# Optimization experiments

Measured on AMD Instinct MI355X. Metric: run time of the kernel, lower is better.

## Reference

```python
import jax, jax.numpy as jnp
import numpy as np

N_HEAD = 12

def fillnan(x):
    return jnp.nan_to_num(x, nan=0.0, posinf=0.0, neginf=0.0)

def setup_inputs() -> dict:
    key = jax.random.key(0)
    k1, k2, k3 = jax.random.split(key, 3)
    B, T, C = 2, 2048, 768
    x = jax.random.normal(k1, (B, T, C), dtype=jnp.float32)
    W_attn = jax.random.normal(k2, (3 * C, C), dtype=jnp.float32) * 0.02
    W_proj = jax.random.normal(k3, (C, C), dtype=jnp.float32) * 0.02
    return {"x": x, "W_attn": W_attn, "W_proj": W_proj}

def reference(x, W_attn, W_proj):
    B, T, C = x.shape
    H = N_HEAD
    D = C // H
    # qkv projection (torch Linear: x @ W^T), then nan-sanitize
    qkv = fillnan(jnp.einsum('btc,fc->btf', x, W_attn))  # [B,T,3C]
    q, k, v = jnp.split(qkv, 3, axis=-1)
    # [B,T,C] -> [B,H,T,D]
    q = q.reshape(B, T, H, D).transpose(0, 2, 1, 3)
    k = k.reshape(B, T, H, D).transpose(0, 2, 1, 3)
    v = v.reshape(B, T, H, D).transpose(0, 2, 1, 3)
    scale = 1.0 / np.sqrt(D).astype(np.float32)
    att = jnp.einsum('bhqd,bhkd->bhqk', q, k) * scale  # [B,H,T,T]
    att = fillnan(att)
    causal = jnp.tril(jnp.ones((T, T), dtype=bool))
    att = jnp.where(causal[None, None], att, -jnp.inf)
    att = jax.nn.softmax(att, axis=-1)
    att = fillnan(att)
    y = jnp.einsum('bhqk,bhkd->bhqd', att, v)  # [B,H,T,D]
    y = fillnan(y)
    y = y.transpose(0, 2, 1, 3).reshape(B, T, C)
    y = fillnan(jnp.einsum('btc,fc->btf', y, W_proj))
    return y
```

## Files before the change

### kernel.cpp

```cpp
#include <hip/hip_runtime.h>

typedef __attribute__((ext_vector_type(8))) short bf16x8;
typedef __attribute__((ext_vector_type(4))) float f32x4;

__device__ __forceinline__ unsigned short f2b(float f) {
  union { float f; unsigned u; } v; v.f = f;
  return (unsigned short)((v.u + 0x7FFFu + ((v.u >> 16) & 1u)) >> 16);
}
__device__ __forceinline__ unsigned short f2b_fast(float f) {
  union { float f; unsigned u; } v; v.f = f;
  return (unsigned short)((v.u + 0x8000u) >> 16);
}

#define XN4   786432
#define WAN4  442368
#define WPN4  147456
__global__ void cvt_all(const float* __restrict__ x, const float* __restrict__ Wa,
                        const float* __restrict__ Wp,
                        unsigned short* __restrict__ xb, unsigned short* __restrict__ Wab,
                        unsigned short* __restrict__ Wpb) {
  int i = blockIdx.x * 256 + threadIdx.x;
  const float* src; unsigned short* dst; int off;
  if (i < XN4)            { src = x;  dst = xb;  off = i; }
  else if (i < XN4 + WAN4){ src = Wa; dst = Wab; off = i - XN4; }
  else                    { src = Wp; dst = Wpb; off = i - XN4 - WAN4; }
  float4 f = reinterpret_cast<const float4*>(src)[off];
  ushort4 o;
  o.x = f2b(f.x); o.y = f2b(f.y); o.z = f2b(f.z); o.w = f2b(f.w);
  reinterpret_cast<ushort4*>(dst)[off] = o;
}

__global__ __launch_bounds__(256, 2)
void gemm_qkv(const unsigned short* __restrict__ A,
              const unsigned short* __restrict__ Bm,
              unsigned short* __restrict__ qb,
              unsigned short* __restrict__ kb_,
              unsigned short* __restrict__ vt) {
  __shared__ unsigned short As[2][128 * 64];
  __shared__ unsigned short Bs[2][128 * 64];
  const int K = 768;
  int tid = threadIdx.x;
  int wave = tid >> 6, lane = tid & 63;
  int quad = lane >> 4, l16 = lane & 15;
  int m0 = blockIdx.x * 128, n0 = blockIdx.y * 128;
  int wm = (wave & 1) * 64, wn = (wave >> 1) * 64;
  bool vswap = (n0 >= 1536);

  int srow = lane >> 3;
  int scol = ((lane & 7) ^ srow) << 3;

  auto stage = [&](int k0, int buf) {
#pragma unroll
    for (int i = 0; i < 4; ++i) {
      int r = wave * 32 + i * 8;
      __builtin_amdgcn_global_load_lds(
          (const __attribute__((address_space(1))) unsigned int*)(A + (size_t)(m0 + r + srow) * K + k0 + scol),
          (__attribute__((address_space(3))) unsigned int*)(&As[buf][r * 64]), 16, 0, 0);
      __builtin_amdgcn_global_load_lds(
          (const __attribute__((address_space(1))) unsigned int*)(Bm + (size_t)(n0 + r + srow) * K + k0 + scol),
          (__attribute__((address_space(3))) unsigned int*)(&Bs[buf][r * 64]), 16, 0, 0);
    }
  };

  f32x4 acc[4][4] = {};
  stage(0, 0);
  int cur = 0;

  for (int k0 = 0; k0 < K; k0 += 64) {
    __syncthreads();
    if (k0 + 64 < K) stage(k0 + 64, cur ^ 1);
#pragma unroll
    for (int kb = 0; kb < 2; ++kb) {
      int ch = (((kb << 2) | quad) ^ (l16 & 7)) << 3;
      bf16x8 af[4], bf[4];
#pragma unroll
      for (int i = 0; i < 4; ++i)
        af[i] = *reinterpret_cast<const bf16x8*>(&As[cur][(wm + i * 16 + l16) * 64 + ch]);
#pragma unroll
      for (int j = 0; j < 4; ++j)
        bf[j] = *reinterpret_cast<const bf16x8*>(&Bs[cur][(wn + j * 16 + l16) * 64 + ch]);
      if (!vswap) {
#pragma unroll
        for (int i = 0; i < 4; ++i)
#pragma unroll
          for (int j = 0; j < 4; ++j)
            acc[i][j] = __builtin_amdgcn_mfma_f32_16x16x32_bf16(af[i], bf[j], acc[i][j], 0, 0, 0);
      } else {
#pragma unroll
        for (int i = 0; i < 4; ++i)
#pragma unroll
          for (int j = 0; j < 4; ++j)
            acc[i][j] = __builtin_amdgcn_mfma_f32_16x16x32_bf16(bf[j], af[i], acc[i][j], 0, 0, 0);
      }
    }
    cur ^= 1;
  }

  const float scale2 = 0.125f * 1.44269504089f;
  if (!vswap) {
#pragma unroll
    for (int i = 0; i < 4; ++i) {
      int mbase = m0 + wm + i * 16 + quad * 4;
#pragma unroll
      for (int j = 0; j < 4; ++j) {
        int f = n0 + wn + j * 16 + l16;
        int which = f / 768;
        int f2 = f - which * 768;
        int h = f2 >> 6, d = f2 & 63;
#pragma unroll
        for (int r = 0; r < 4; ++r) {
          int m = mbase + r;
          int b = m >> 11, t = m & 2047;
          int bh = b * 12 + h;
          if (which == 0) qb[((size_t)(bh * 2048 + t)) * 64 + d] = f2b(acc[i][j][r] * scale2);
          else            kb_[((size_t)(bh * 2048 + t)) * 64 + d] = f2b(acc[i][j][r]);
        }
      }
    }
  } else {
#pragma unroll
    for (int j = 0; j < 4; ++j) {
      int fbase = n0 + wn + j * 16 + quad * 4 - 1536;
#pragma unroll
      for (int i = 0; i < 4; ++i) {
        int t_g = m0 + wm + i * 16 + l16;
        int b = t_g >> 11, t = t_g & 2047;
#pragma unroll
        for (int r = 0; r < 4; ++r) {
          int f2 = fbase + r;
          int h = f2 >> 6, d = f2 & 63;
          int bh = b * 12 + h;
          vt[((size_t)(bh * 64 + d)) * 2048 + t] = f2b(acc[i][j][r]);
        }
      }
    }
  }
}

#define CK 256

__global__ __launch_bounds__(256, 3)
void attn_part(const unsigned short* __restrict__ Qb,
               const unsigned short* __restrict__ Kb,
               const unsigned short* __restrict__ Vt,
               float* __restrict__ Oacc, float* __restrict__ Lacc) {
  __shared__ unsigned short Ks[2][64 * 64];
  __shared__ unsigned short Vs[2][64 * 64];
  __shared__ unsigned short P[4 * 32 * 64];
  const int T = 2048, D = 64;
  int wave = threadIdx.x >> 6, lane = threadIdx.x & 63;
  int quad = lane >> 4, l16 = lane & 15;

  int flat = blockIdx.x;
  int xcd = flat & 7;
  int ix = flat >> 3;
  int bh = xcd * 3 + ix / 72;
  int r = ix % 72;
  int b = 15;
#pragma unroll
  for (int i = 0; i < 16; ++i) {
    int nb = (i >> 1) + 1;
    if (r < nb) { b = i; break; }
    r -= nb;
  }
  int c = r;
  int q0 = b * 128;
  int qrow = q0 + wave * 32;
  int kbeg = c * CK;
  int kend = kbeg + CK; if (kend > q0 + 128) kend = q0 + 128;

  const unsigned short* Qp = Qb + (size_t)bh * T * D;
  const unsigned short* Kp = Kb + (size_t)bh * T * D;
  const unsigned short* Vp = Vt + (size_t)bh * D * T;
  unsigned short* Pw = P + wave * 32 * 64;

  int srow = lane >> 3;
  int scol = ((lane & 7) ^ srow) << 3;

  auto stage = [&](int k0, int buf) {
#pragma unroll
    for (int i = 0; i < 2; ++i) {
      int rr = wave * 16 + i * 8;
      __builtin_amdgcn_global_load_lds(
          (const __attribute__((address_space(1))) unsigned int*)(Kp + (size_t)(k0 + rr + srow) * D + scol),
          (__attribute__((address_space(3))) unsigned int*)(&Ks[buf][rr * 64]), 16, 0, 0);
      __builtin_amdgcn_global_load_lds(
          (const __attribute__((address_space(1))) unsigned int*)(Vp + (size_t)(rr + srow) * T + k0 + scol),
          (__attribute__((address_space(3))) unsigned int*)(&Vs[buf][rr * 64]), 16, 0, 0);
    }
  };

  bf16x8 aq[2][2];
#pragma unroll
  for (int qi = 0; qi < 2; ++qi)
#pragma unroll
    for (int cc = 0; cc < 2; ++cc)
      aq[qi][cc] = *reinterpret_cast<const bf16x8*>(
          Qp + (qrow + qi * 16 + l16) * D + cc * 32 + quad * 8);

  bf16x8 ones;
#pragma unroll
  for (int e = 0; e < 8; ++e) ones[e] = (short)0x3F80;

  f32x4 o[2][4] = {};
  f32x4 lacc[2] = {};
  int pswr = (l16 & 7) ^ (l16 >> 3);

  stage(kbeg, 0);
  int cur = 0;

  for (int k0 = kbeg; k0 < kend; k0 += 64) {
    __syncthreads();
    if (k0 + 64 < kend) stage(k0 + 64, cur ^ 1);

    if (k0 <= qrow + 31) {
      f32x4 sacc[2][4] = {};
#pragma unroll
      for (int nt = 0; nt < 4; ++nt) {
        bf16x8 bk0 = *reinterpret_cast<const bf16x8*>(&Ks[cur][(nt * 16 + l16) * 64 + ((quad ^ (l16 & 7)) << 3)]);
        bf16x8 bk1 = *reinterpret_cast<const bf16x8*>(&Ks[cur][(nt * 16 + l16) * 64 + (((4 | quad) ^ (l16 & 7)) << 3)]);
#pragma unroll
        for (int qi = 0; qi < 2; ++qi) {
          sacc[qi][nt] = __builtin_amdgcn_mfma_f32_16x16x32_bf16(aq[qi][0], bk0, sacc[qi][nt], 0, 0, 0);
          sacc[qi][nt] = __builtin_amdgcn_mfma_f32_16x16x32_bf16(aq[qi][1], bk1, sacc[qi][nt], 0, 0, 0);
        }
      }

      if (k0 + 63 > qrow) {
#pragma unroll
        for (int qi = 0; qi < 2; ++qi)
#pragma unroll
          for (int nt = 0; nt < 4; ++nt) {
            int col = k0 + nt * 16 + l16;
#pragma unroll
            for (int rr = 0; rr < 4; ++rr) {
              int row = qrow + qi * 16 + quad * 4 + rr;
              sacc[qi][nt][rr] = (col <= row) ? sacc[qi][nt][rr] : -1e30f;
            }
          }
      }
#pragma unroll
      for (int qi = 0; qi < 2; ++qi)
#pragma unroll
        for (int nt = 0; nt < 4; ++nt)
#pragma unroll
          for (int rr = 0; rr < 4; ++rr)
            sacc[qi][nt][rr] = exp2f(sacc[qi][nt][rr]);

#pragma unroll
      for (int qi = 0; qi < 2; ++qi)
#pragma unroll
        for (int rr = 0; rr < 4; ++rr) {
          int prow = qi * 16 + quad * 4 + rr;
          int psw = (prow & 7) ^ ((prow >> 3) & 1);
#pragma unroll
          for (int nt = 0; nt < 4; ++nt)
            Pw[prow * 64 + (((nt * 2 + (l16 >> 3)) ^ psw) << 3) + (l16 & 7)] = f2b_fast(sacc[qi][nt][rr]);
        }
      __asm__ volatile("s_waitcnt lgkmcnt(0)" ::: "memory");

      bf16x8 vf[4][2];
#pragma unroll
      for (int dt = 0; dt < 4; ++dt) {
        vf[dt][0] = *reinterpret_cast<const bf16x8*>(&Vs[cur][(dt * 16 + l16) * 64 + ((quad ^ (l16 & 7)) << 3)]);
        vf[dt][1] = *reinterpret_cast<const bf16x8*>(&Vs[cur][(dt * 16 + l16) * 64 + (((4 | quad) ^ (l16 & 7)) << 3)]);
      }
#pragma unroll
      for (int qi = 0; qi < 2; ++qi) {
        bf16x8 ap0 = *reinterpret_cast<const bf16x8*>(Pw + (qi * 16 + l16) * 64 + ((quad ^ pswr) << 3));
        bf16x8 ap1 = *reinterpret_cast<const bf16x8*>(Pw + (qi * 16 + l16) * 64 + (((4 | quad) ^ pswr) << 3));
#pragma unroll
        for (int dt = 0; dt < 4; ++dt) {
          o[qi][dt] = __builtin_amdgcn_mfma_f32_16x16x32_bf16(ap0, vf[dt][0], o[qi][dt], 0, 0, 0);
          o[qi][dt] = __builtin_amdgcn_mfma_f32_16x16x32_bf16(ap1, vf[dt][1], o[qi][dt], 0, 0, 0);
        }
        lacc[qi] = __builtin_amdgcn_mfma_f32_16x16x32_bf16(ap0, ones, lacc[qi], 0, 0, 0);
        lacc[qi] = __builtin_amdgcn_mfma_f32_16x16x32_bf16(ap1, ones, lacc[qi], 0, 0, 0);
      }
      __asm__ volatile("" ::: "memory");
    }
    cur ^= 1;
  }

#pragma unroll
  for (int qi = 0; qi < 2; ++qi)
#pragma unroll
    for (int dt = 0; dt < 4; ++dt)
#pragma unroll
      for (int rr = 0; rr < 4; ++rr) {
        int row = qrow + qi * 16 + quad * 4 + rr;
        atomicAdd(&Oacc[((size_t)(bh * T + row)) * 64 + dt * 16 + l16], o[qi][dt][rr]);
      }
  if (l16 == 0) {
#pragma unroll
    for (int qi = 0; qi < 2; ++qi)
#pragma unroll
      for (int rr = 0; rr < 4; ++rr)
        atomicAdd(&Lacc[bh * T + qrow + qi * 16 + quad * 4 + rr], lacc[qi][rr]);
  }
}

__global__ __launch_bounds__(256, 2)
void gemm_proj(const float* __restrict__ Oacc, const float* __restrict__ Lacc,
               const unsigned short* __restrict__ Wpb, float* __restrict__ out) {
  __shared__ unsigned short As[2][64 * 64];
  __shared__ unsigned short Bs[2][128 * 64];
  int tid = threadIdx.x;
  int wave = tid >> 6, lane = tid & 63;
  int quad = lane >> 4, l16 = lane & 15;
  int m0 = blockIdx.x * 64, n0 = blockIdx.y * 128;
  int wm = (wave & 1) * 32, wn = (wave >> 1) * 64;

  int srow = lane >> 3;
  int scol = ((lane & 7) ^ srow) << 3;

  int arow = tid >> 2;
  int acg = (tid & 3) * 2;
  int t_g = m0 + arow;
  int bb = t_g >> 11, tt = t_g & 2047;
  int asw = arow & 7;

  auto stageB = [&](int k0, int buf) {
#pragma unroll
    for (int i = 0; i < 4; ++i) {
      int r = wave * 32 + i * 8;
      __builtin_amdgcn_global_load_lds(
          (const __attribute__((address_space(1))) unsigned int*)(Wpb + (size_t)(n0 + r + srow) * 768 + k0 + scol),
          (__attribute__((address_space(3))) unsigned int*)(&Bs[buf][r * 64]), 16, 0, 0);
    }
  };
  auto loadA = [&](int k0, float4* a, float& rl) {
    int h = k0 >> 6;
    const float* arp = Oacc + ((size_t)((bb * 12 + h) * 2048 + tt)) * 64 + acg * 8;
    rl = 1.0f / Lacc[(bb * 12 + h) * 2048 + tt];
    a[0] = reinterpret_cast<const float4*>(arp)[0];
    a[1] = reinterpret_cast<const float4*>(arp)[1];
    a[2] = reinterpret_cast<const float4*>(arp)[2];
    a[3] = reinterpret_cast<const float4*>(arp)[3];
  };
  auto writeA = [&](const float4* a, float rl, int buf) {
    bf16x8 p0, p1;
    p0[0] = (short)f2b(a[0].x * rl); p0[1] = (short)f2b(a[0].y * rl);
    p0[2] = (short)f2b(a[0].z * rl); p0[3] = (short)f2b(a[0].w * rl);
    p0[4] = (short)f2b(a[1].x * rl); p0[5] = (short)f2b(a[1].y * rl);
    p0[6] = (short)f2b(a[1].z * rl); p0[7] = (short)f2b(a[1].w * rl);
    p1[0] = (short)f2b(a[2].x * rl); p1[1] = (short)f2b(a[2].y * rl);
    p1[2] = (short)f2b(a[2].z * rl); p1[3] = (short)f2b(a[2].w * rl);
    p1[4] = (short)f2b(a[3].x * rl); p1[5] = (short)f2b(a[3].y * rl);
    p1[6] = (short)f2b(a[3].z * rl); p1[7] = (short)f2b(a[3].w * rl);
    *reinterpret_cast<bf16x8*>(&As[buf][arow * 64 + ((acg ^ asw) << 3)]) = p0;
    *reinterpret_cast<bf16x8*>(&As[buf][arow * 64 + (((acg + 1) ^ asw) << 3)]) = p1;
  };

  f32x4 acc[2][4] = {};

  float4 aP[4], aN[4];
  float rlP, rlN;
  stageB(0, 0);
  loadA(0, aP, rlP);
  loadA(64, aN, rlN);
  writeA(aP, rlP, 0);
  int cur = 0;

  for (int k0 = 0; k0 < 768; k0 += 64) {
    __syncthreads();
    if (k0 + 64 < 768) {
      stageB(k0 + 64, cur ^ 1);
      writeA(aN, rlN, cur ^ 1);
      if (k0 + 128 < 768) loadA(k0 + 128, aN, rlN);
    }
#pragma unroll
    for (int kb = 0; kb < 2; ++kb) {
      int ch = (((kb << 2) | quad) ^ (l16 & 7)) << 3;
      bf16x8 af[2], bf[4];
#pragma unroll
      for (int i = 0; i < 2; ++i)
        af[i] = *reinterpret_cast<const bf16x8*>(&As[cur][(wm + i * 16 + l16) * 64 + ch]);
#pragma unroll
      for (int j = 0; j < 4; ++j)
        bf[j] = *reinterpret_cast<const bf16x8*>(&Bs[cur][(wn + j * 16 + l16) * 64 + ch]);
#pragma unroll
      for (int i = 0; i < 2; ++i)
#pragma unroll
        for (int j = 0; j < 4; ++j)
          acc[i][j] = __builtin_amdgcn_mfma_f32_16x16x32_bf16(af[i], bf[j], acc[i][j], 0, 0, 0);
    }
    cur ^= 1;
  }

#pragma unroll
  for (int i = 0; i < 2; ++i) {
    int mbase = m0 + wm + i * 16 + quad * 4;
#pragma unroll
    for (int j = 0; j < 4; ++j) {
      int col = n0 + wn + j * 16 + l16;
#pragma unroll
      for (int r = 0; r < 4; ++r)
        out[(size_t)(mbase + r) * 768 + col] = acc[i][j][r];
    }
  }
}

extern "C" void kernel_launch(void* const* d_in, const int* in_sizes, int n_in,
                              void* d_out, int out_size, void* d_ws, size_t ws_size,
                              hipStream_t stream) {
  const float* x  = (const float*)d_in[0];
  const float* Wa = (const float*)d_in[1];
  const float* Wp = (const float*)d_in[2];
  float* out = (float*)d_out;

  unsigned short* ws = (unsigned short*)d_ws;
  unsigned short* xb  = ws;
  unsigned short* Wab = xb  + 3145728;
  unsigned short* Wpb = Wab + 1769472;
  unsigned short* Qb  = Wpb + 589824;
  unsigned short* Kb  = Qb  + 3145728;
  unsigned short* Vt  = Kb  + 3145728;
  float*          Oacc = (float*)(Vt + 3145728);
  float*          Lacc = Oacc + 3145728;

  hipMemsetAsync(Oacc, 0, (3145728 + 49152) * sizeof(float), stream);

  cvt_all<<<(XN4 + WAN4 + WPN4) / 256, 256, 0, stream>>>(x, Wa, Wp, xb, Wab, Wpb);

  gemm_qkv<<<dim3(32, 18), 256, 0, stream>>>(xb, Wab, Qb, Kb, Vt);

  attn_part<<<1728, 256, 0, stream>>>(Qb, Kb, Vt, Oacc, Lacc);

  gemm_proj<<<dim3(64, 6), 256, 0, stream>>>(Oacc, Lacc, Wpb, out);
}
```

Before: 180.8 us.

## Restructure attention into independent per-wave 16-row tasks with direct global K/V loads

The attention kernel now gives each wave its own 16-query-row × 256-key chunk. Each wave loads K and V fragments straight from global memory into registers, which removes the shared-memory staging, double buffering and block-wide barriers. Blocks become 512 threads with 8 independent waves, so causal work is spread more finely and there is no intra-block sync. The memset of the accumulators is folded into the conversion kernel to save a launch. In exchange, K/V reuse across waves through LDS is lost, and there are more global loads and atomics per output row.

```diff
diff --git a/kernel.cpp b/kernel.cpp
--- a/kernel.cpp
+++ b/kernel.cpp
@@ -15,11 +15,18 @@
 #define XN4   786432
 #define WAN4  442368
 #define WPN4  147456
+#define CVTN  1376256
+#define ZN4   798720
 __global__ void cvt_all(const float* __restrict__ x, const float* __restrict__ Wa,
                         const float* __restrict__ Wp,
                         unsigned short* __restrict__ xb, unsigned short* __restrict__ Wab,
-                        unsigned short* __restrict__ Wpb) {
+                        unsigned short* __restrict__ Wpb, float* __restrict__ Oacc) {
   int i = blockIdx.x * 256 + threadIdx.x;
+  if (i >= CVTN) {
+    int z = i - CVTN;
+    reinterpret_cast<float4*>(Oacc)[z] = make_float4(0.f, 0.f, 0.f, 0.f);
+    return;
+  }
   const float* src; unsigned short* dst; int off;
   if (i < XN4)            { src = x;  dst = xb;  off = i; }
   else if (i < XN4 + WAN4){ src = Wa; dst = Wab; off = i - XN4; }
@@ -137,166 +144,114 @@
   }
 }
 
-#define CK 256
-
-__global__ __launch_bounds__(256, 3)
+#define AT_LDP 72
+
+__global__ __launch_bounds__(512, 4)
 void attn_part(const unsigned short* __restrict__ Qb,
                const unsigned short* __restrict__ Kb,
                const unsigned short* __restrict__ Vt,
                float* __restrict__ Oacc, float* __restrict__ Lacc) {
-  __shared__ unsigned short Ks[2][64 * 64];
-  __shared__ unsigned short Vs[2][64 * 64];
-  __shared__ unsigned short P[4 * 32 * 64];
+  __shared__ unsigned short P[8 * 16 * AT_LDP];
   const int T = 2048, D = 64;
   int wave = threadIdx.x >> 6, lane = threadIdx.x & 63;
   int quad = lane >> 4, l16 = lane & 15;
 
-  int flat = blockIdx.x;
-  int xcd = flat & 7;
-  int ix = flat >> 3;
+  int blk = blockIdx.x;
+  int xcd = blk & 7;
+  int ix = blk >> 3;
   int bh = xcd * 3 + ix / 72;
-  int r = ix % 72;
-  int b = 15;
-#pragma unroll
-  for (int i = 0; i < 16; ++i) {
-    int nb = (i >> 1) + 1;
-    if (r < nb) { b = i; break; }
-    r -= nb;
-  }
-  int c = r;
-  int q0 = b * 128;
-  int qrow = q0 + wave * 32;
-  int kbeg = c * CK;
-  int kend = kbeg + CK; if (kend > q0 + 128) kend = q0 + 128;
+  int r = (ix % 72) * 8 + wave;
+  int qt = 0, c = 0;
+#pragma unroll
+  for (int G = 0; G < 8; ++G) {
+    int cnt = 16 * (G + 1);
+    if (r >= cnt) { r -= cnt; }
+    else { qt = G * 16 + r / (G + 1); c = r % (G + 1); break; }
+  }
+  int qrow = qt * 16;
+  int kbeg = c * 256;
+  int kend = kbeg + 256; if (kend > qrow + 16) kend = qrow + 16;
 
   const unsigned short* Qp = Qb + (size_t)bh * T * D;
   const unsigned short* Kp = Kb + (size_t)bh * T * D;
   const unsigned short* Vp = Vt + (size_t)bh * D * T;
-  unsigned short* Pw = P + wave * 32 * 64;
-
-  int srow = lane >> 3;
-  int scol = ((lane & 7) ^ srow) << 3;
-
-  auto stage = [&](int k0, int buf) {
-#pragma unroll
-    for (int i = 0; i < 2; ++i) {
-      int rr = wave * 16 + i * 8;
-      __builtin_amdgcn_global_load_lds(
-          (const __attribute__((address_space(1))) unsigned int*)(Kp + (size_t)(k0 + rr + srow) * D + scol),
-          (__attribute__((address_space(3))) unsigned int*)(&Ks[buf][rr * 64]), 16, 0, 0);
-      __builtin_amdgcn_global_load_lds(
-          (const __attribute__((address_space(1))) unsigned int*)(Vp + (size_t)(rr + srow) * T + k0 + scol),
-          (__attribute__((address_space(3))) unsigned int*)(&Vs[buf][rr * 64]), 16, 0, 0);
-    }
-  };
-
-  bf16x8 aq[2][2];
-#pragma unroll
-  for (int qi = 0; qi < 2; ++qi)
-#pragma unroll
-    for (int cc = 0; cc < 2; ++cc)
-      aq[qi][cc] = *reinterpret_cast<const bf16x8*>(
-          Qp + (qrow + qi * 16 + l16) * D + cc * 32 + quad * 8);
+  unsigned short* Pw = P + wave * 16 * AT_LDP;
+
+  bf16x8 aq[2];
+#pragma unroll
+  for (int cc = 0; cc < 2; ++cc)
+    aq[cc] = *reinterpret_cast<const bf16x8*>(Qp + (qrow + l16) * D + cc * 32 + quad * 8);
 
   bf16x8 ones;
 #pragma unroll
   for (int e = 0; e < 8; ++e) ones[e] = (short)0x3F80;
 
-  f32x4 o[2][4] = {};
-  f32x4 lacc[2] = {};
-  int pswr = (l16 & 7) ^ (l16 >> 3);
-
-  stage(kbeg, 0);
-  int cur = 0;
+  f32x4 o[4] = {};
+  f32x4 lacc = {};
 
   for (int k0 = kbeg; k0 < kend; k0 += 64) {
-    __syncthreads();
-    if (k0 + 64 < kend) stage(k0 + 64, cur ^ 1);
-
-    if (k0 <= qrow + 31) {
-      f32x4 sacc[2][4] = {};
-#pragma unroll
-      for (int nt = 0; nt < 4; ++nt) {
-        bf16x8 bk0 = *reinterpret_cast<const bf16x8*>(&Ks[cur][(nt * 16 + l16) * 64 + ((quad ^ (l16 & 7)) << 3)]);
-        bf16x8 bk1 = *reinterpret_cast<const bf16x8*>(&Ks[cur][(nt * 16 + l16) * 64 + (((4 | quad) ^ (l16 & 7)) << 3)]);
-#pragma unroll
-        for (int qi = 0; qi < 2; ++qi) {
-          sacc[qi][nt] = __builtin_amdgcn_mfma_f32_16x16x32_bf16(aq[qi][0], bk0, sacc[qi][nt], 0, 0, 0);
-          sacc[qi][nt] = __builtin_amdgcn_mfma_f32_16x16x32_bf16(aq[qi][1], bk1, sacc[qi][nt], 0, 0, 0);
-        }
+    bf16x8 kf[4][2];
+#pragma unroll
+    for (int nt = 0; nt < 4; ++nt) {
+      const unsigned short* kr = Kp + (size_t)(k0 + nt * 16 + l16) * D + quad * 8;
+      kf[nt][0] = *reinterpret_cast<const bf16x8*>(kr);
+      kf[nt][1] = *reinterpret_cast<const bf16x8*>(kr + 32);
+    }
+    f32x4 sacc[4] = {};
+#pragma unroll
+    for (int nt = 0; nt < 4; ++nt) {
+      sacc[nt] = __builtin_amdgcn_mfma_f32_16x16x32_bf16(aq[0], kf[nt][0], sacc[nt], 0, 0, 0);
+      sacc[nt] = __builtin_amdgcn_mfma_f32_16x16x32_bf16(aq[1], kf[nt][1], sacc[nt], 0, 0, 0);
+    }
+    bf16x8 vf[4][2];
+#pragma unroll
+    for (int dt = 0; dt < 4; ++dt) {
+      const unsigned short* vr = Vp + (size_t)(dt * 16 + l16) * T + k0 + quad * 8;
+      vf[dt][0] = *reinterpret_cast<const bf16x8*>(vr);
+      vf[dt][1] = *reinterpret_cast<const bf16x8*>(vr + 32);
+    }
+
+#pragma unroll
+    for (int nt = 0; nt < 4; ++nt) {
+      int col = k0 + nt * 16 + l16;
+#pragma unroll
+      for (int rr = 0; rr < 4; ++rr) {
+        int row = qrow + quad * 4 + rr;
+        float s = (col <= row) ? sacc[nt][rr] : -1e30f;
+        sacc[nt][rr] = exp2f(s);
       }
-
-      if (k0 + 63 > qrow) {
-#pragma unroll
-        for (int qi = 0; qi < 2; ++qi)
-#pragma unroll
-          for (int nt = 0; nt < 4; ++nt) {
-            int col = k0 + nt * 16 + l16;
-#pragma unroll
-            for (int rr = 0; rr < 4; ++rr) {
-              int row = qrow + qi * 16 + quad * 4 + rr;
-              sacc[qi][nt][rr] = (col <= row) ? sacc[qi][nt][rr] : -1e30f;
-            }
-          }
-      }
-#pragma unroll
-      for (int qi = 0; qi < 2; ++qi)
-#pragma unroll
-        for (int nt = 0; nt < 4; ++nt)
-#pragma unroll
-          for (int rr = 0; rr < 4; ++rr)
-            sacc[qi][nt][rr] = exp2f(sacc[qi][nt][rr]);
-
-#pragma unroll
-      for (int qi = 0; qi < 2; ++qi)
-#pragma unroll
-        for (int rr = 0; rr < 4; ++rr) {
-          int prow = qi * 16 + quad * 4 + rr;
-          int psw = (prow & 7) ^ ((prow >> 3) & 1);
-#pragma unroll
-          for (int nt = 0; nt < 4; ++nt)
-            Pw[prow * 64 + (((nt * 2 + (l16 >> 3)) ^ psw) << 3) + (l16 & 7)] = f2b_fast(sacc[qi][nt][rr]);
-        }
-      __asm__ volatile("s_waitcnt lgkmcnt(0)" ::: "memory");
-
-      bf16x8 vf[4][2];
-#pragma unroll
-      for (int dt = 0; dt < 4; ++dt) {
-        vf[dt][0] = *reinterpret_cast<const bf16x8*>(&Vs[cur][(dt * 16 + l16) * 64 + ((quad ^ (l16 & 7)) << 3)]);
-        vf[dt][1] = *reinterpret_cast<const bf16x8*>(&Vs[cur][(dt * 16 + l16) * 64 + (((4 | quad) ^ (l16 & 7)) << 3)]);
-      }
-#pragma unroll
-      for (int qi = 0; qi < 2; ++qi) {
-        bf16x8 ap0 = *reinterpret_cast<const bf16x8*>(Pw + (qi * 16 + l16) * 64 + ((quad ^ pswr) << 3));
-        bf16x8 ap1 = *reinterpret_cast<const bf16x8*>(Pw + (qi * 16 + l16) * 64 + (((4 | quad) ^ pswr) << 3));
-#pragma unroll
-        for (int dt = 0; dt < 4; ++dt) {
-          o[qi][dt] = __builtin_amdgcn_mfma_f32_16x16x32_bf16(ap0, vf[dt][0], o[qi][dt], 0, 0, 0);
-          o[qi][dt] = __builtin_amdgcn_mfma_f32_16x16x32_bf16(ap1, vf[dt][1], o[qi][dt], 0, 0, 0);
-        }
-        lacc[qi] = __builtin_amdgcn_mfma_f32_16x16x32_bf16(ap0, ones, lacc[qi], 0, 0, 0);
-        lacc[qi] = __builtin_amdgcn_mfma_f32_16x16x32_bf16(ap1, ones, lacc[qi], 0, 0, 0);
-      }
-      __asm__ volatile("" ::: "memory");
-    }
-    cur ^= 1;
-  }
-
-#pragma unroll
-  for (int qi = 0; qi < 2; ++qi)
-#pragma unroll
-    for (int dt = 0; dt < 4; ++dt)
-#pragma unroll
-      for (int rr = 0; rr < 4; ++rr) {
-        int row = qrow + qi * 16 + quad * 4 + rr;
-        atomicAdd(&Oacc[((size_t)(bh * T + row)) * 64 + dt * 16 + l16], o[qi][dt][rr]);
-      }
+    }
+
+#pragma unroll
+    for (int nt = 0; nt < 4; ++nt)
+#pragma unroll
+      for (int rr = 0; rr < 4; ++rr)
+        Pw[(quad * 4 + rr) * AT_LDP + nt * 16 + l16] = f2b_fast(sacc[nt][rr]);
+    __asm__ volatile("s_waitcnt lgkmcnt(0)" ::: "memory");
+
+    bf16x8 ap0 = *reinterpret_cast<const bf16x8*>(Pw + l16 * AT_LDP + quad * 8);
+    bf16x8 ap1 = *reinterpret_cast<const bf16x8*>(Pw + l16 * AT_LDP + 32 + quad * 8);
+#pragma unroll
+    for (int dt = 0; dt < 4; ++dt) {
+      o[dt] = __builtin_amdgcn_mfma_f32_16x16x32_bf16(ap0, vf[dt][0], o[dt], 0, 0, 0);
+      o[dt] = __builtin_amdgcn_mfma_f32_16x16x32_bf16(ap1, vf[dt][1], o[dt], 0, 0, 0);
+    }
+    lacc = __builtin_amdgcn_mfma_f32_16x16x32_bf16(ap0, ones, lacc, 0, 0, 0);
+    lacc = __builtin_amdgcn_mfma_f32_16x16x32_bf16(ap1, ones, lacc, 0, 0, 0);
+    __asm__ volatile("" ::: "memory");
+  }
+
+#pragma unroll
+  for (int dt = 0; dt < 4; ++dt)
+#pragma unroll
+    for (int rr = 0; rr < 4; ++rr) {
+      int row = qrow + quad * 4 + rr;
+      atomicAdd(&Oacc[((size_t)(bh * T + row)) * 64 + dt * 16 + l16], o[dt][rr]);
+    }
   if (l16 == 0) {
 #pragma unroll
-    for (int qi = 0; qi < 2; ++qi)
-#pragma unroll
-      for (int rr = 0; rr < 4; ++rr)
-        atomicAdd(&Lacc[bh * T + qrow + qi * 16 + quad * 4 + rr], lacc[qi][rr]);
+    for (int rr = 0; rr < 4; ++rr)
+      atomicAdd(&Lacc[bh * T + qrow + quad * 4 + rr], lacc[rr]);
   }
 }
 
@@ -419,13 +374,11 @@
   float*          Oacc = (float*)(Vt + 3145728);
   float*          Lacc = Oacc + 3145728;
 
-  hipMemsetAsync(Oacc, 0, (3145728 + 49152) * sizeof(float), stream);
-
-  cvt_all<<<(XN4 + WAN4 + WPN4) / 256, 256, 0, stream>>>(x, Wa, Wp, xb, Wab, Wpb);
+  cvt_all<<<(CVTN + ZN4) / 256, 256, 0, stream>>>(x, Wa, Wp, xb, Wab, Wpb, Oacc);
 
   gemm_qkv<<<dim3(32, 18), 256, 0, stream>>>(xb, Wab, Qb, Kb, Vt);
 
-  attn_part<<<1728, 256, 0, stream>>>(Qb, Kb, Vt, Oacc, Lacc);
+  attn_part<<<1728, 512, 0, stream>>>(Qb, Kb, Vt, Oacc, Lacc);
 
   gemm_proj<<<dim3(64, 6), 256, 0, stream>>>(Oacc, Lacc, Wpb, out);
 }
```

Result: slower. 225.4 us (+24.7%).
